# Optimization experiments

Hardware: AMD Instinct MI355X
Metric: run time of the kernel (lower is better)

The kernel has to match this reference:

```python
import jax, jax.numpy as jnp
import numpy as np

PALACE_N = 64   # base palace mask size
PALACE_BLOCK = 8  # 8 palaces of 8 positions each


def _palace_base():
    # base 64x64 mask: 1.0 within a palace (8x8 diagonal blocks), 0.5 across palaces
    pid = jnp.arange(PALACE_N) // PALACE_BLOCK
    intra = pid[:, None] == pid[None, :]
    return jnp.where(intra, 1.0, 0.5).astype(jnp.float32)


def _get_mask(T, inter_palace_weight):
    # tile base mask by index modulo 64 (matches mask[i % 64, j % 64])
    base = _palace_base()
    ii = jnp.arange(T) % PALACE_N
    base_T = base[ii[:, None], ii[None, :]]            # [T, T]
    intra = (base_T == 1.0).astype(jnp.float32)
    inter = (base_T < 1.0).astype(jnp.float32)
    return intra + jax.nn.sigmoid(inter_palace_weight) * inter


def setup_inputs() -> dict:
    key = jax.random.key(0)
    ks = jax.random.split(key, 5)
    B, T, D = 4, 2048, 1024
    x = jax.random.normal(ks[0], (B, T, D), dtype=jnp.float32)
    s = 1.0 / np.sqrt(D)
    Wq = jax.random.normal(ks[1], (D, D), dtype=jnp.float32) * s
    Wk = jax.random.normal(ks[2], (D, D), dtype=jnp.float32) * s
    Wv = jax.random.normal(ks[3], (D, D), dtype=jnp.float32) * s
    inter_palace_weight = jnp.float32(0.1)
    return {"x": x, "Wq": Wq, "Wk": Wk, "Wv": Wv,
            "inter_palace_weight": inter_palace_weight}


def reference(x, Wq, Wk, Wv, inter_palace_weight):
    B, T, D = x.shape
    H = 16
    hd = D // H
    scale = hd ** -0.5
    pmask = _get_mask(T, inter_palace_weight)          # [T, T]
    # torch Linear: x @ W.T
    q = (x @ Wq.T).reshape(B, T, H, hd)
    k = (x @ Wk.T).reshape(B, T, H, hd)
    v = (x @ Wv.T).reshape(B, T, H, hd)
    attn = jnp.einsum('bqhd,bkhd->bhqk', q, k) * scale
    attn = attn * pmask[None, None, :, :]
    attn = jax.nn.softmax(attn, axis=-1)
    attn = jnp.nan_to_num(attn, nan=0.0)
    out = jnp.einsum('bhqk,bkhd->bqhd', attn, v)
    return out.reshape(B, T, D)
```

## Files before the change

### kernel.cpp

```cpp
#include <hip/hip_runtime.h>

typedef unsigned short u16;
typedef unsigned int u32;
typedef short bf16x8 __attribute__((ext_vector_type(8)));
typedef float f32x4 __attribute__((ext_vector_type(4)));
typedef u32 u32x4 __attribute__((ext_vector_type(4)));

#define AS_GLOBAL __attribute__((address_space(1)))
#define AS_LDS __attribute__((address_space(3)))

__device__ __forceinline__ void async16(const void* g, void* l) {
  __builtin_amdgcn_global_load_lds((const AS_GLOBAL u32*)g, (AS_LDS u32*)l, 16, 0, 0);
}

__device__ __forceinline__ u16 f2bf(float f) {
  u32 u = __builtin_bit_cast(u32, f);
  u += 0x7FFFu + ((u >> 16) & 1u);
  return (u16)(u >> 16);
}

__device__ __forceinline__ u32 pk2bf(float lo, float hi) {
  return __builtin_amdgcn_perm(__builtin_bit_cast(u32, hi),
                               __builtin_bit_cast(u32, lo), 0x07060302u);
}

__device__ __forceinline__ float fexp2(float x) {
#if __has_builtin(__builtin_amdgcn_exp2f)
  return __builtin_amdgcn_exp2f(x);
#else
  return exp2f(x);
#endif
}

__global__ __launch_bounds__(256) void cvt_all(const float* __restrict__ x,
                                               const float* __restrict__ wq,
                                               const float* __restrict__ wk,
                                               const float* __restrict__ wv,
                                               u16* __restrict__ xb,
                                               u16* __restrict__ wb) {
  const int blk = blockIdx.x;
  const float* src;
  u16* dst;
  int i;
  if (blk < 8192) {
    src = x; dst = xb; i = blk * 256 + threadIdx.x;
  } else if (blk < 9216) {
    src = wq; dst = wb; i = (blk - 8192) * 256 + threadIdx.x;
  } else if (blk < 10240) {
    src = wk; dst = wb + 1048576; i = (blk - 9216) * 256 + threadIdx.x;
  } else {
    src = wv; dst = wb + 2097152; i = (blk - 10240) * 256 + threadIdx.x;
  }
  float4 f = reinterpret_cast<const float4*>(src)[i];
  ushort4 o;
  o.x = f2bf(f.x); o.y = f2bf(f.y); o.z = f2bf(f.z); o.w = f2bf(f.w);
  reinterpret_cast<ushort4*>(dst)[i] = o;
}

__global__ __launch_bounds__(256, 3) void qkv_gemm(const u16* __restrict__ X,
                                                   const u16* __restrict__ W,
                                                   u16* __restrict__ O) {
  const int z = blockIdx.z;
  const u16* Wz = W + (size_t)z * (1024 * 1024);
  u16* Oz = O + (size_t)z * (8192 * 1024);

  __shared__ __align__(16) u16 As[2][128 * 32];
  __shared__ __align__(16) u16 Bs[2][128 * 32];

  const int t = threadIdx.x;
  const int lane = t & 63, w = t >> 6, quad = lane >> 4, lq = lane & 15;
  const int wm = (w >> 1) * 64, wn = (w & 1) * 64;
  const size_t m0 = (size_t)blockIdx.x * 128;
  const int n0 = blockIdx.y * 128;
  const int srow = t >> 2, sseg = (t & 3) * 8;

  f32x4 acc[4][4];
#pragma unroll
  for (int i = 0; i < 4; ++i)
#pragma unroll
    for (int j = 0; j < 4; ++j) acc[i][j] = f32x4{0.f, 0.f, 0.f, 0.f};

  const u16* ga = X + (m0 + srow) * 1024 + sseg;
  const u16* gb = Wz + (size_t)(n0 + srow) * 1024 + sseg;

  async16(ga, &As[0][srow * 32 + sseg]);
  async16(ga + 64 * 1024, &As[0][(64 + srow) * 32 + sseg]);
  async16(gb, &Bs[0][srow * 32 + sseg]);
  async16(gb + 64 * 1024, &Bs[0][(64 + srow) * 32 + sseg]);

  for (int kt = 0; kt < 32; ++kt) {
    const int cur = kt & 1;
    __syncthreads();
    if (kt < 31) {
      const int k1 = (kt + 1) * 32;
      async16(ga + k1, &As[cur ^ 1][srow * 32 + sseg]);
      async16(ga + 64 * 1024 + k1, &As[cur ^ 1][(64 + srow) * 32 + sseg]);
      async16(gb + k1, &Bs[cur ^ 1][srow * 32 + sseg]);
      async16(gb + 64 * 1024 + k1, &Bs[cur ^ 1][(64 + srow) * 32 + sseg]);
    }
    bf16x8 af[4], bfr[4];
#pragma unroll
    for (int i = 0; i < 4; ++i)
      af[i] = *reinterpret_cast<const bf16x8*>(&As[cur][(wm + i * 16 + lq) * 32 + quad * 8]);
#pragma unroll
    for (int j = 0; j < 4; ++j)
      bfr[j] = *reinterpret_cast<const bf16x8*>(&Bs[cur][(wn + j * 16 + lq) * 32 + quad * 8]);
#pragma unroll
    for (int i = 0; i < 4; ++i)
#pragma unroll
      for (int j = 0; j < 4; ++j)
        acc[i][j] = __builtin_amdgcn_mfma_f32_16x16x32_bf16(af[i], bfr[j], acc[i][j], 0, 0, 0);
  }

#pragma unroll
  for (int i = 0; i < 4; ++i) {
#pragma unroll
    for (int j = 0; j < 4; ++j) {
      const int n = n0 + wn + j * 16 + lq;
      const int hh = n >> 6, d = n & 63;
#pragma unroll
      for (int r = 0; r < 4; ++r) {
        const size_t m = m0 + wm + i * 16 + quad * 4 + r;
        const size_t bb = m >> 11, tt = m & 2047;
        if (z != 2)
          Oz[((bb * 16 + hh) * 2048 + tt) * 64 + d] = f2bf(acc[i][j][r]);
        else
          Oz[((bb * 16 + hh) * 64 + d) * 2048 + tt] = f2bf(acc[i][j][r]);
      }
    }
  }
}

__global__ __launch_bounds__(256, 2) void palace_attn(const u16* __restrict__ Q,
                                                      const u16* __restrict__ K,
                                                      const u16* __restrict__ Vt,
                                                      float* __restrict__ out,
                                                      const float* __restrict__ wptr) {
  const int bh = blockIdx.x, qt = blockIdx.y;
  const int h = bh & 15, b = bh >> 4;
  const size_t base = (size_t)bh * (2048 * 64);

  __shared__ __align__(16) u16 Ks[2][64 * 64];
  __shared__ __align__(16) u16 Vs[2][64 * 64];

  const int t = threadIdx.x;
  const int w = t >> 6, lane = t & 63, quad = lane >> 4, lq = lane & 15;
  const int lq3 = lq >> 3;
  const int swk = (lq & 3) | (((lq >> 2) & 1) << 2);
  const int swv = (lq & 3) | (lq3 << 2);
  const float sig = 1.f / (1.f + __expf(-wptr[0]));
  const float Ci = 0.125f * 1.44269504f;
  const float Co = Ci * sig;
  const float MC = 14.4269504f;

  float cft[2][4];
#pragma unroll
  for (int half = 0; half < 2; ++half)
#pragma unroll
    for (int qg = 0; qg < 4; ++qg)
      cft[half][qg] = (half * 4 + quad == qg * 2 + lq3) ? Ci : Co;

  bf16x8 qf[4][2];
#pragma unroll
  for (int qg = 0; qg < 4; ++qg)
#pragma unroll
    for (int kc = 0; kc < 2; ++kc)
      qf[qg][kc] = *reinterpret_cast<const bf16x8*>(
          Q + base + (size_t)(qt * 256 + w * 64 + qg * 16 + lq) * 64 + kc * 32 + quad * 8);

  int ko[2], vo[2];
#pragma unroll
  for (int r = 0; r < 2; ++r) {
    const int slot = r * 256 + t;
    const int row = slot >> 3;
    const int sr = (row & 3) | (((row >> 3) & 1) << 2);
    const int cl = (slot & 7) ^ sr;
    ko[r] = row * 64 + cl * 8;
    vo[r] = row * 2048 + cl * 8;
  }

  f32x4 O[4][4];
  f32x4 Lacc[4];
#pragma unroll
  for (int qg = 0; qg < 4; ++qg) {
    Lacc[qg] = f32x4{0.f, 0.f, 0.f, 0.f};
#pragma unroll
    for (int dg = 0; dg < 4; ++dg) O[qg][dg] = f32x4{0.f, 0.f, 0.f, 0.f};
  }

  const short oneb = (short)0x3F80;
  const bf16x8 ones8 = {oneb, oneb, oneb, oneb, oneb, oneb, oneb, oneb};

  {
    const u16* kgp = K + base;
    const u16* vgp = Vt + base;
    async16(kgp + ko[0], &Ks[0][(w * 64) * 8]);
    async16(kgp + ko[1], &Ks[0][(256 + w * 64) * 8]);
    async16(vgp + vo[0], &Vs[0][(w * 64) * 8]);
    async16(vgp + vo[1], &Vs[0][(256 + w * 64) * 8]);
  }

  for (int kt = 0; kt < 32; ++kt) {
    const int cur = kt & 1;
    __syncthreads();
    if (kt < 31) {
      const u16* kgp = K + base + (size_t)(kt + 1) * 4096;
      const u16* vgp = Vt + base + (size_t)(kt + 1) * 64;
      const int nb = cur ^ 1;
      async16(kgp + ko[0], &Ks[nb][(w * 64) * 8]);
      async16(kgp + ko[1], &Ks[nb][(256 + w * 64) * 8]);
      async16(vgp + vo[0], &Vs[nb][(w * 64) * 8]);
      async16(vgp + vo[1], &Vs[nb][(256 + w * 64) * 8]);
    }

#pragma unroll
    for (int half = 0; half < 2; ++half) {
      const int rb = half * 32 + ((lq >> 2) << 3) + (lq & 3);
      bf16x8 kf[2][2];
#pragma unroll
      for (int kg2 = 0; kg2 < 2; ++kg2) {
        const int krow = rb + kg2 * 4;
        kf[kg2][0] = *reinterpret_cast<const bf16x8*>(
            &Ks[cur][krow * 64 + (quad ^ swk) * 8]);
        kf[kg2][1] = *reinterpret_cast<const bf16x8*>(
            &Ks[cur][krow * 64 + ((quad + 4) ^ swk) * 8]);
      }

      bf16x8 vbf[4];
#pragma unroll
      for (int dg = 0; dg < 4; ++dg)
        vbf[dg] = *reinterpret_cast<const bf16x8*>(
            &Vs[cur][(dg * 16 + lq) * 64 + ((half * 4 + quad) ^ swv) * 8]);

#pragma unroll
      for (int qg = 0; qg < 4; ++qg) {
        f32x4 z0 = {0.f, 0.f, 0.f, 0.f}, z1 = {0.f, 0.f, 0.f, 0.f};
        z0 = __builtin_amdgcn_mfma_f32_16x16x32_bf16(kf[0][0], qf[qg][0], z0, 0, 0, 0);
        z0 = __builtin_amdgcn_mfma_f32_16x16x32_bf16(kf[0][1], qf[qg][1], z0, 0, 0, 0);
        z1 = __builtin_amdgcn_mfma_f32_16x16x32_bf16(kf[1][0], qf[qg][0], z1, 0, 0, 0);
        z1 = __builtin_amdgcn_mfma_f32_16x16x32_bf16(kf[1][1], qf[qg][1], z1, 0, 0, 0);

        const float cf = cft[half][qg];
        const float p0 = fexp2(__builtin_fmaf(z0[0], cf, -MC));
        const float p1 = fexp2(__builtin_fmaf(z0[1], cf, -MC));
        const float p2 = fexp2(__builtin_fmaf(z0[2], cf, -MC));
        const float p3 = fexp2(__builtin_fmaf(z0[3], cf, -MC));
        const float p4 = fexp2(__builtin_fmaf(z1[0], cf, -MC));
        const float p5 = fexp2(__builtin_fmaf(z1[1], cf, -MC));
        const float p6 = fexp2(__builtin_fmaf(z1[2], cf, -MC));
        const float p7 = fexp2(__builtin_fmaf(z1[3], cf, -MC));

        u32x4 pk;
        pk.x = pk2bf(p0, p1);
        pk.y = pk2bf(p2, p3);
        pk.z = pk2bf(p4, p5);
        pk.w = pk2bf(p6, p7);
        const bf16x8 pa = __builtin_bit_cast(bf16x8, pk);

        Lacc[qg] = __builtin_amdgcn_mfma_f32_16x16x32_bf16(pa, ones8, Lacc[qg], 0, 0, 0);
#pragma unroll
        for (int dg = 0; dg < 4; ++dg)
          O[qg][dg] = __builtin_amdgcn_mfma_f32_16x16x32_bf16(pa, vbf[dg], O[qg][dg], 0, 0, 0);
      }
    }
  }

#pragma unroll
  for (int qg = 0; qg < 4; ++qg) {
#pragma unroll
    for (int r = 0; r < 4; ++r) {
      const float iv = 1.f / Lacc[qg][r];
      const size_t trow = (size_t)(qt * 256 + w * 64 + qg * 16 + quad * 4 + r);
      float* op = out + ((size_t)b * 2048 + trow) * 1024 + h * 64 + lq;
#pragma unroll
      for (int dg = 0; dg < 4; ++dg) op[dg * 16] = O[qg][dg][r] * iv;
    }
  }
}

extern "C" void kernel_launch(void* const* d_in, const int* in_sizes, int n_in,
                              void* d_out, int out_size, void* d_ws, size_t ws_size,
                              hipStream_t stream) {
  (void)in_sizes; (void)n_in; (void)out_size; (void)ws_size;
  const float* x = (const float*)d_in[0];
  const float* Wq = (const float*)d_in[1];
  const float* Wk = (const float*)d_in[2];
  const float* Wv = (const float*)d_in[3];
  const float* wip = (const float*)d_in[4];
  float* out = (float*)d_out;

  u16* xb = (u16*)d_ws;
  u16* wb = xb + 8388608;
  u16* qb = wb + 3145728;
  u16* kb = qb + 8388608;
  u16* vb = kb + 8388608;

  cvt_all<<<11264, 256, 0, stream>>>(x, Wq, Wk, Wv, xb, wb);
  qkv_gemm<<<dim3(64, 8, 3), 256, 0, stream>>>(xb, wb, qb);
  palace_attn<<<dim3(64, 8, 1), 256, 0, stream>>>(qb, kb, vb, out, wip);
}
```

Measured before the change: 244.3 us.

## Restructure QKV GEMM into 128x256x64 tiles with swizzled LDS and vmcnt pipelining

The QKV projection GEMM now uses 512-thread blocks computing 128x256 output tiles with K-step 64 instead of 128x128 with K-step 32. LDS tiles are XOR-swizzled to avoid bank conflicts, prefetch is overlapped with compute using an explicit partial vmcnt wait, and MFMA sections are given raised scheduling priority. The aim is better operand reuse, fewer barriers per FLOP and fewer LDS conflicts. The cost is more LDS per block (96 KB), which limits occupancy.

Result: no change. 245.5 us (+0.5%).

```diff
diff --git a/kernel.cpp b/kernel.cpp
--- a/kernel.cpp
+++ b/kernel.cpp
@@ -57,22 +57,36 @@
   reinterpret_cast<ushort4*>(dst)[i] = o;
 }
 
-__global__ __launch_bounds__(256, 3) void qkv_gemm(const u16* __restrict__ X,
+__global__ __launch_bounds__(512, 2) void qkv_gemm(const u16* __restrict__ X,
                                                    const u16* __restrict__ W,
                                                    u16* __restrict__ O) {
   const int z = blockIdx.z;
   const u16* Wz = W + (size_t)z * (1024 * 1024);
   u16* Oz = O + (size_t)z * (8192 * 1024);
 
-  __shared__ __align__(16) u16 As[2][128 * 32];
-  __shared__ __align__(16) u16 Bs[2][128 * 32];
+  __shared__ __align__(16) u16 As[2][128 * 64];
+  __shared__ __align__(16) u16 Bs[2][256 * 64];
 
   const int t = threadIdx.x;
   const int lane = t & 63, w = t >> 6, quad = lane >> 4, lq = lane & 15;
-  const int wm = (w >> 1) * 64, wn = (w & 1) * 64;
+  const int wm = (w >> 2) * 64, wn = (w & 3) * 64;
+  const int sw = lq & 7;
   const size_t m0 = (size_t)blockIdx.x * 128;
-  const int n0 = blockIdx.y * 128;
-  const int srow = t >> 2, sseg = (t & 3) * 8;
+  const int n0 = blockIdx.y * 256;
+
+  int aoff[2], boff[4];
+#pragma unroll
+  for (int j = 0; j < 2; ++j) {
+    const int s = j * 512 + t, row = s >> 3, c = (s & 7) ^ (row & 7);
+    aoff[j] = row * 1024 + c * 8;
+  }
+#pragma unroll
+  for (int j = 0; j < 4; ++j) {
+    const int s = j * 512 + t, row = s >> 3, c = (s & 7) ^ (row & 7);
+    boff[j] = row * 1024 + c * 8;
+  }
+  const u16* gA = X + m0 * 1024;
+  const u16* gB = Wz + (size_t)n0 * 1024;
 
   f32x4 acc[4][4];
 #pragma unroll
@@ -80,37 +94,79 @@
 #pragma unroll
     for (int j = 0; j < 4; ++j) acc[i][j] = f32x4{0.f, 0.f, 0.f, 0.f};
 
-  const u16* ga = X + (m0 + srow) * 1024 + sseg;
-  const u16* gb = Wz + (size_t)(n0 + srow) * 1024 + sseg;
-
-  async16(ga, &As[0][srow * 32 + sseg]);
-  async16(ga + 64 * 1024, &As[0][(64 + srow) * 32 + sseg]);
-  async16(gb, &Bs[0][srow * 32 + sseg]);
-  async16(gb + 64 * 1024, &Bs[0][(64 + srow) * 32 + sseg]);
-
-  for (int kt = 0; kt < 32; ++kt) {
+  auto stage = [&](int kt, int nb) {
+    const u16* ga = gA + kt * 64;
+    const u16* gb = gB + kt * 64;
+    async16(gb + boff[0], &Bs[nb][(0 * 512 + t) * 8]);
+    async16(gb + boff[1], &Bs[nb][(1 * 512 + t) * 8]);
+    async16(gb + boff[2], &Bs[nb][(2 * 512 + t) * 8]);
+    async16(gb + boff[3], &Bs[nb][(3 * 512 + t) * 8]);
+    async16(ga + aoff[0], &As[nb][(0 * 512 + t) * 8]);
+    async16(ga + aoff[1], &As[nb][(1 * 512 + t) * 8]);
+  };
+
+  auto compute_tile = [&](int cur) {
+    bf16x8 Bf[4][2];
+#pragma unroll
+    for (int j = 0; j < 4; ++j)
+#pragma unroll
+      for (int ks = 0; ks < 2; ++ks)
+        Bf[j][ks] = *reinterpret_cast<const bf16x8*>(
+            &Bs[cur][(wn + j * 16 + lq) * 64 + ((ks * 4 + quad) ^ sw) * 8]);
+    {
+      bf16x8 Af[2][2];
+#pragma unroll
+      for (int i = 0; i < 2; ++i)
+#pragma unroll
+        for (int ks = 0; ks < 2; ++ks)
+          Af[i][ks] = *reinterpret_cast<const bf16x8*>(
+              &As[cur][(wm + i * 16 + lq) * 64 + ((ks * 4 + quad) ^ sw) * 8]);
+      __builtin_amdgcn_s_setprio(1);
+#pragma unroll
+      for (int i = 0; i < 2; ++i)
+#pragma unroll
+        for (int j = 0; j < 4; ++j) {
+          acc[i][j] = __builtin_amdgcn_mfma_f32_16x16x32_bf16(Af[i][0], Bf[j][0], acc[i][j], 0, 0, 0);
+          acc[i][j] = __builtin_amdgcn_mfma_f32_16x16x32_bf16(Af[i][1], Bf[j][1], acc[i][j], 0, 0, 0);
+        }
+      __builtin_amdgcn_s_setprio(0);
+    }
+    {
+      bf16x8 Af[2][2];
+#pragma unroll
+      for (int i = 0; i < 2; ++i)
+#pragma unroll
+        for (int ks = 0; ks < 2; ++ks)
+          Af[i][ks] = *reinterpret_cast<const bf16x8*>(
+              &As[cur][(wm + (i + 2) * 16 + lq) * 64 + ((ks * 4 + quad) ^ sw) * 8]);
+      __builtin_amdgcn_s_setprio(1);
+#pragma unroll
+      for (int i = 0; i < 2; ++i)
+#pragma unroll
+        for (int j = 0; j < 4; ++j) {
+          acc[i + 2][j] = __builtin_amdgcn_mfma_f32_16x16x32_bf16(Af[i][0], Bf[j][0], acc[i + 2][j], 0, 0, 0);
+          acc[i + 2][j] = __builtin_amdgcn_mfma_f32_16x16x32_bf16(Af[i][1], Bf[j][1], acc[i + 2][j], 0, 0, 0);
+        }
+      __builtin_amdgcn_s_setprio(0);
+    }
+  };
+
+  stage(0, 0);
+
+  for (int kt = 0; kt < 15; ++kt) {
     const int cur = kt & 1;
-    __syncthreads();
-    if (kt < 31) {
-      const int k1 = (kt + 1) * 32;
-      async16(ga + k1, &As[cur ^ 1][srow * 32 + sseg]);
-      async16(ga + 64 * 1024 + k1, &As[cur ^ 1][(64 + srow) * 32 + sseg]);
-      async16(gb + k1, &Bs[cur ^ 1][srow * 32 + sseg]);
-      async16(gb + 64 * 1024 + k1, &Bs[cur ^ 1][(64 + srow) * 32 + sseg]);
-    }
-    bf16x8 af[4], bfr[4];
-#pragma unroll
-    for (int i = 0; i < 4; ++i)
-      af[i] = *reinterpret_cast<const bf16x8*>(&As[cur][(wm + i * 16 + lq) * 32 + quad * 8]);
-#pragma unroll
-    for (int j = 0; j < 4; ++j)
-      bfr[j] = *reinterpret_cast<const bf16x8*>(&Bs[cur][(wn + j * 16 + lq) * 32 + quad * 8]);
-#pragma unroll
-    for (int i = 0; i < 4; ++i)
-#pragma unroll
-      for (int j = 0; j < 4; ++j)
-        acc[i][j] = __builtin_amdgcn_mfma_f32_16x16x32_bf16(af[i], bfr[j], acc[i][j], 0, 0, 0);
-  }
+    stage(kt + 1, cur ^ 1);
+    asm volatile("s_waitcnt vmcnt(6)" ::: "memory");
+    __builtin_amdgcn_s_barrier();
+    __builtin_amdgcn_sched_barrier(0);
+    compute_tile(cur);
+    __builtin_amdgcn_sched_barrier(0);
+    __builtin_amdgcn_s_barrier();
+  }
+  asm volatile("s_waitcnt vmcnt(0)" ::: "memory");
+  __builtin_amdgcn_s_barrier();
+  __builtin_amdgcn_sched_barrier(0);
+  compute_tile(1);
 
 #pragma unroll
   for (int i = 0; i < 4; ++i) {
@@ -296,6 +352,6 @@
   u16* vb = kb + 8388608;
 
   cvt_all<<<11264, 256, 0, stream>>>(x, Wq, Wk, Wv, xb, wb);
-  qkv_gemm<<<dim3(64, 8, 3), 256, 0, stream>>>(xb, wb, qb);
+  qkv_gemm<<<dim3(64, 4, 3), 512, 0, stream>>>(xb, wb, qb);
   palace_attn<<<dim3(64, 8, 1), 256, 0, stream>>>(qb, kb, vb, out, wip);
 }
```

## Double K-tile depth in QKV GEMM and XOR-swizzle LDS layout

Applied to the files above, without the earlier changes.

The QKV projection GEMM now stages 64-wide K tiles instead of 32-wide ones, which halves the number of loop iterations and barriers. The LDS layout is XOR-swizzled so the fragment reads avoid bank conflicts. LDS per block doubles, so launch bounds drop from 3 to 2 blocks per SM. This trades occupancy for fewer syncs and conflict-free shared-memory reads.

After: 246.9 us. No clear change (+1.0%).

```diff
diff --git a/kernel.cpp b/kernel.cpp
--- a/kernel.cpp
+++ b/kernel.cpp
@@ -57,22 +57,31 @@
   reinterpret_cast<ushort4*>(dst)[i] = o;
 }
 
-__global__ __launch_bounds__(256, 3) void qkv_gemm(const u16* __restrict__ X,
+__global__ __launch_bounds__(256, 2) void qkv_gemm(const u16* __restrict__ X,
                                                    const u16* __restrict__ W,
                                                    u16* __restrict__ O) {
   const int z = blockIdx.z;
   const u16* Wz = W + (size_t)z * (1024 * 1024);
   u16* Oz = O + (size_t)z * (8192 * 1024);
 
-  __shared__ __align__(16) u16 As[2][128 * 32];
-  __shared__ __align__(16) u16 Bs[2][128 * 32];
+  __shared__ __align__(16) u16 As[2][128 * 64];
+  __shared__ __align__(16) u16 Bs[2][128 * 64];
 
   const int t = threadIdx.x;
   const int lane = t & 63, w = t >> 6, quad = lane >> 4, lq = lane & 15;
   const int wm = (w >> 1) * 64, wn = (w & 1) * 64;
+  const int sw = lq & 7;
   const size_t m0 = (size_t)blockIdx.x * 128;
   const int n0 = blockIdx.y * 128;
-  const int srow = t >> 2, sseg = (t & 3) * 8;
+
+  int off[4];
+#pragma unroll
+  for (int j = 0; j < 4; ++j) {
+    const int s = j * 256 + t, row = s >> 3, c = (s & 7) ^ (row & 7);
+    off[j] = row * 1024 + c * 8;
+  }
+  const u16* gA = X + m0 * 1024;
+  const u16* gB = Wz + (size_t)n0 * 1024;
 
   f32x4 acc[4][4];
 #pragma unroll
@@ -80,36 +89,41 @@
 #pragma unroll
     for (int j = 0; j < 4; ++j) acc[i][j] = f32x4{0.f, 0.f, 0.f, 0.f};
 
-  const u16* ga = X + (m0 + srow) * 1024 + sseg;
-  const u16* gb = Wz + (size_t)(n0 + srow) * 1024 + sseg;
-
-  async16(ga, &As[0][srow * 32 + sseg]);
-  async16(ga + 64 * 1024, &As[0][(64 + srow) * 32 + sseg]);
-  async16(gb, &Bs[0][srow * 32 + sseg]);
-  async16(gb + 64 * 1024, &Bs[0][(64 + srow) * 32 + sseg]);
-
-  for (int kt = 0; kt < 32; ++kt) {
+  auto stage = [&](int kt, int nb) {
+    const u16* ga = gA + kt * 64;
+    const u16* gb = gB + kt * 64;
+#pragma unroll
+    for (int j = 0; j < 4; ++j)
+      async16(ga + off[j], &As[nb][(j * 256 + t) * 8]);
+#pragma unroll
+    for (int j = 0; j < 4; ++j)
+      async16(gb + off[j], &Bs[nb][(j * 256 + t) * 8]);
+  };
+
+  stage(0, 0);
+
+  for (int kt = 0; kt < 16; ++kt) {
     const int cur = kt & 1;
     __syncthreads();
-    if (kt < 31) {
-      const int k1 = (kt + 1) * 32;
-      async16(ga + k1, &As[cur ^ 1][srow * 32 + sseg]);
-      async16(ga + 64 * 1024 + k1, &As[cur ^ 1][(64 + srow) * 32 + sseg]);
-      async16(gb + k1, &Bs[cur ^ 1][srow * 32 + sseg]);
-      async16(gb + 64 * 1024 + k1, &Bs[cur ^ 1][(64 + srow) * 32 + sseg]);
-    }
-    bf16x8 af[4], bfr[4];
+    if (kt < 15) stage(kt + 1, cur ^ 1);
+
+    bf16x8 Af[4][2], Bf[4][2];
 #pragma unroll
     for (int i = 0; i < 4; ++i)
-      af[i] = *reinterpret_cast<const bf16x8*>(&As[cur][(wm + i * 16 + lq) * 32 + quad * 8]);
-#pragma unroll
-    for (int j = 0; j < 4; ++j)
-      bfr[j] = *reinterpret_cast<const bf16x8*>(&Bs[cur][(wn + j * 16 + lq) * 32 + quad * 8]);
+#pragma unroll
+      for (int ks = 0; ks < 2; ++ks) {
+        Af[i][ks] = *reinterpret_cast<const bf16x8*>(
+            &As[cur][(wm + i * 16 + lq) * 64 + ((ks * 4 + quad) ^ sw) * 8]);
+        Bf[i][ks] = *reinterpret_cast<const bf16x8*>(
+            &Bs[cur][(wn + i * 16 + lq) * 64 + ((ks * 4 + quad) ^ sw) * 8]);
+      }
 #pragma unroll
     for (int i = 0; i < 4; ++i)
 #pragma unroll
-      for (int j = 0; j < 4; ++j)
-        acc[i][j] = __builtin_amdgcn_mfma_f32_16x16x32_bf16(af[i], bfr[j], acc[i][j], 0, 0, 0);
+      for (int j = 0; j < 4; ++j) {
+        acc[i][j] = __builtin_amdgcn_mfma_f32_16x16x32_bf16(Af[i][0], Bf[j][0], acc[i][j], 0, 0, 0);
+        acc[i][j] = __builtin_amdgcn_mfma_f32_16x16x32_bf16(Af[i][1], Bf[j][1], acc[i][j], 0, 0, 0);
+      }
   }
 
 #pragma unroll
```
